# Kernel tuning notes

Hardware: AMD Instinct MI355X
Metric: run time of the kernel (lower is better)

The kernel has to match this reference:

```python
import jax, jax.numpy as jnp
import numpy as np

B, D_IN, D_H = 262144, 128, 128
PROJ_EPS = 1e-5  # ball projection epsilon (c = 1.0)


def _norm(x):
    return jnp.linalg.norm(x, axis=-1, keepdims=True)


def logmap0(x):
    # atanh(||x||) * x / ||x||, safe at 0 (c = 1)
    n = _norm(x)
    ns = jnp.where(n == 0, 0.5, n)
    return jnp.where(n == 0, jnp.zeros_like(x), jnp.arctanh(ns) * x / ns)


def expmap0(v):
    # tanh(||v||) * v / ||v||, safe at 0 (c = 1)
    n = _norm(v)
    ns = jnp.where(n == 0, 1.0, n)
    return jnp.where(n == 0, jnp.zeros_like(v), jnp.tanh(ns) * v / ns)


def proj(x):
    # clip back inside the unit Poincare ball
    n = _norm(x)
    maxnorm = 1.0 - PROJ_EPS
    ns = jnp.where(n == 0, 1.0, n)
    return jnp.where(n > maxnorm, x / ns * maxnorm, x)


def setup_inputs() -> dict:
    key = jax.random.key(0)
    ks = jax.random.split(key, 8)
    scale = 0.03  # keep points well inside the ball: ||x|| ~ 0.03*sqrt(128) ~ 0.34
    x = scale * jax.random.normal(ks[0], (B, D_IN), dtype=jnp.float32)
    h = scale * jax.random.normal(ks[1], (B, D_H), dtype=jnp.float32)
    fan_in = D_IN + D_H
    w_std = 1.0 / np.sqrt(fan_in)
    Wr = w_std * jax.random.normal(ks[2], (fan_in, D_H), dtype=jnp.float32)
    br = w_std * jax.random.normal(ks[3], (D_H,), dtype=jnp.float32)
    Wz = w_std * jax.random.normal(ks[4], (fan_in, D_H), dtype=jnp.float32)
    bz = w_std * jax.random.normal(ks[5], (D_H,), dtype=jnp.float32)
    Wh = w_std * jax.random.normal(ks[6], (fan_in, D_H), dtype=jnp.float32)
    bh = w_std * jax.random.normal(ks[7], (D_H,), dtype=jnp.float32)
    return {"x": x, "h": h, "Wr": Wr, "br": br, "Wz": Wz, "bz": bz, "Wh": Wh, "bh": bh}


def reference(x, h, Wr, br, Wz, bz, Wh, bh):
    x_tan = logmap0(x)            # [B, D_IN]
    h_tan = logmap0(h)            # [B, D_H]
    xh = jnp.concatenate([x_tan, h_tan], axis=1)  # [B, D_IN+D_H]
    r = jax.nn.sigmoid(xh @ Wr + br)
    z = jax.nn.sigmoid(xh @ Wz + bz)
    xh_reset = jnp.concatenate([x_tan, r * h_tan], axis=1)
    h_tilde = jnp.tanh(xh_reset @ Wh + bh)
    h_new_tan = (1.0 - z) * h_tan + z * h_tilde
    return proj(expmap0(h_new_tan))  # [B, D_H]
```

## Files before the change

kernel.cpp:

```cpp
#include <hip/hip_runtime.h>

typedef __attribute__((ext_vector_type(4))) float f32x4;
typedef __attribute__((ext_vector_type(8))) short bf16x8;
typedef __attribute__((ext_vector_type(4))) short bf16x4;

#define D 128
#define BM 64

__device__ __forceinline__ unsigned short f2bf(float f){
  union { float f; unsigned int i; } c; c.f = f;
  unsigned int i = c.i;
  i += 0x7fffu + ((i >> 16) & 1u);
  return (unsigned short)(i >> 16);
}
__device__ __forceinline__ float bf2f(unsigned short u){
  union { float f; unsigned int i; } c; c.i = ((unsigned int)u) << 16; return c.f;
}
__device__ __forceinline__ float sigmoid_f(float t){
  return 1.0f / (1.0f + __expf(-t));
}
__device__ __forceinline__ float tanh_f(float t){
  t = fminf(fmaxf(t, -20.0f), 20.0f);
  float e = __expf(2.0f * t);
  return (e - 1.0f) / (e + 1.0f);
}

__global__ void prep_weights(const float* __restrict__ Wr, const float* __restrict__ Wz,
                             const float* __restrict__ Wh, unsigned short* __restrict__ wp)
{
  int w = blockIdx.x >> 6;
  int f = blockIdx.x & 63;
  int l = threadIdx.x;
  const float* src = (w == 0) ? Wr : ((w == 1) ? Wz : Wh);
  int nf = f >> 3, kk = f & 7;
  int col = nf * 16 + (l & 15);
  int k0  = kk * 32 + (l >> 4) * 8;
  unsigned short* dst = wp + w * 32768 + (f * 64 + l) * 8;
#pragma unroll
  for (int j = 0; j < 8; ++j)
    dst[j] = f2bf(src[(k0 + j) * D + col]);
}

__global__ __launch_bounds__(256, 3) void gru_fused(
    const float* __restrict__ x, const float* __restrict__ h,
    const float* __restrict__ brp, const float* __restrict__ bzp, const float* __restrict__ bhp,
    const unsigned short* __restrict__ wp, float* __restrict__ out)
{
  __shared__ __align__(16) unsigned char SMEM[BM * 512 + BM * 256];
  unsigned char* A1 = SMEM;
  unsigned char* A2 = SMEM + BM * 512;
  float* HN = (float*)SMEM;

  const int tid = threadIdx.x;
  const int w   = tid >> 6;
  const int l   = tid & 63;
  const int l15 = l & 15;
  const int lq  = l >> 4;
  const size_t row0 = (size_t)blockIdx.x * BM;

  {
    const int row = tid >> 2;
    const int q   = tid & 3;
    const f32x4* xr = (const f32x4*)(x + (row0 + row) * D);
    const f32x4* hr = (const f32x4*)(h + (row0 + row) * D);
    f32x4 v[8];
    float ss = 0.f;
#pragma unroll
    for (int j = 0; j < 8; ++j){
      v[j] = xr[j * 4 + q];
      ss += v[j][0]*v[j][0] + v[j][1]*v[j][1] + v[j][2]*v[j][2] + v[j][3]*v[j][3];
    }
    ss += __shfl_xor(ss, 1, 64);
    ss += __shfl_xor(ss, 2, 64);
    float n = sqrtf(ss);
    float s = (n > 1e-20f) ? (0.5f * __logf((1.f + n) / (1.f - n)) / n) : 1.f;
#pragma unroll
    for (int j = 0; j < 8; ++j){
      unsigned int byte = (unsigned)(row * 512 + (4 * j + q) * 8) ^ (unsigned)((row & 7) << 4);
      bf16x4 pk;
      pk[0] = (short)f2bf(v[j][0] * s); pk[1] = (short)f2bf(v[j][1] * s);
      pk[2] = (short)f2bf(v[j][2] * s); pk[3] = (short)f2bf(v[j][3] * s);
      *(bf16x4*)(A1 + byte) = pk;
    }
    ss = 0.f;
#pragma unroll
    for (int j = 0; j < 8; ++j){
      v[j] = hr[j * 4 + q];
      ss += v[j][0]*v[j][0] + v[j][1]*v[j][1] + v[j][2]*v[j][2] + v[j][3]*v[j][3];
    }
    ss += __shfl_xor(ss, 1, 64);
    ss += __shfl_xor(ss, 2, 64);
    n = sqrtf(ss);
    s = (n > 1e-20f) ? (0.5f * __logf((1.f + n) / (1.f - n)) / n) : 1.f;
#pragma unroll
    for (int j = 0; j < 8; ++j){
      unsigned int byte = (unsigned)(row * 512 + 256 + (4 * j + q) * 8) ^ (unsigned)((row & 7) << 4);
      bf16x4 pk;
      pk[0] = (short)f2bf(v[j][0] * s); pk[1] = (short)f2bf(v[j][1] * s);
      pk[2] = (short)f2bf(v[j][2] * s); pk[3] = (short)f2bf(v[j][3] * s);
      *(bf16x4*)(A1 + byte) = pk;
    }
  }
  __syncthreads();

  const unsigned short* pwr = wp + w * 8192;
  const unsigned short* pwz = wp + 32768 + w * 8192;

  f32x4 accr0[4], accr1[4], accz0[4], accz1[4];
#pragma unroll
  for (int m = 0; m < 4; ++m){ accr0[m] = 0; accr1[m] = 0; accz0[m] = 0; accz1[m] = 0; }

#pragma unroll 2
  for (int kk = 0; kk < 8; ++kk){
    const bf16x8 br0f = *(const bf16x8*)(pwr + kk * 512 + l * 8);
    const bf16x8 br1f = *(const bf16x8*)(pwr + 4096 + kk * 512 + l * 8);
    const bf16x8 bz0f = *(const bf16x8*)(pwz + kk * 512 + l * 8);
    const bf16x8 bz1f = *(const bf16x8*)(pwz + 4096 + kk * 512 + l * 8);
#pragma unroll
    for (int m = 0; m < 4; ++m){
      const int row = m * 16 + l15;
      unsigned int byte = (unsigned)(row * 512 + (kk * 32 + lq * 8) * 2) ^ (unsigned)((row & 7) << 4);
      const bf16x8 a = *(const bf16x8*)(A1 + byte);
      accr0[m] = __builtin_amdgcn_mfma_f32_16x16x32_bf16(a, br0f, accr0[m], 0, 0, 0);
      accr1[m] = __builtin_amdgcn_mfma_f32_16x16x32_bf16(a, br1f, accr1[m], 0, 0, 0);
      accz0[m] = __builtin_amdgcn_mfma_f32_16x16x32_bf16(a, bz0f, accz0[m], 0, 0, 0);
      accz1[m] = __builtin_amdgcn_mfma_f32_16x16x32_bf16(a, bz1f, accz1[m], 0, 0, 0);
    }
  }

  const int cb = w * 32 + l15;
  const float br0v = brp[cb], br1v = brp[cb + 16];
  const float bz0v = bzp[cb], bz1v = bzp[cb + 16];
  f32x4 zk0[4], zk1[4];
#pragma unroll
  for (int m = 0; m < 4; ++m){
#pragma unroll
    for (int reg = 0; reg < 4; ++reg){
      const int row = m * 16 + lq * 4 + reg;
      const unsigned int swz = (unsigned)((row & 7) << 4);
      {
        float rv = sigmoid_f(accr0[m][reg] + br0v);
        zk0[m][reg] = sigmoid_f(accz0[m][reg] + bz0v);
        float ht = bf2f(*(const unsigned short*)(A1 + ((unsigned)(row * 512 + (128 + cb) * 2) ^ swz)));
        *(unsigned short*)(A2 + ((unsigned)(row * 256 + cb * 2) ^ swz)) = f2bf(rv * ht);
      }
      {
        float rv = sigmoid_f(accr1[m][reg] + br1v);
        zk1[m][reg] = sigmoid_f(accz1[m][reg] + bz1v);
        float ht = bf2f(*(const unsigned short*)(A1 + ((unsigned)(row * 512 + (128 + cb + 16) * 2) ^ swz)));
        *(unsigned short*)(A2 + ((unsigned)(row * 256 + (cb + 16) * 2) ^ swz)) = f2bf(rv * ht);
      }
    }
  }
  __syncthreads();

  const unsigned short* pwh = wp + 65536 + w * 8192;
  f32x4 ac0[4], ac1[4];
#pragma unroll
  for (int m = 0; m < 4; ++m){ ac0[m] = 0; ac1[m] = 0; }

#pragma unroll 2
  for (int kk = 0; kk < 4; ++kk){
    const bf16x8 b0 = *(const bf16x8*)(pwh + kk * 512 + l * 8);
    const bf16x8 b1 = *(const bf16x8*)(pwh + 4096 + kk * 512 + l * 8);
#pragma unroll
    for (int m = 0; m < 4; ++m){
      const int row = m * 16 + l15;
      unsigned int byte = (unsigned)(row * 512 + (kk * 32 + lq * 8) * 2) ^ (unsigned)((row & 7) << 4);
      const bf16x8 a = *(const bf16x8*)(A1 + byte);
      ac0[m] = __builtin_amdgcn_mfma_f32_16x16x32_bf16(a, b0, ac0[m], 0, 0, 0);
      ac1[m] = __builtin_amdgcn_mfma_f32_16x16x32_bf16(a, b1, ac1[m], 0, 0, 0);
    }
  }
#pragma unroll 2
  for (int kk = 4; kk < 8; ++kk){
    const bf16x8 b0 = *(const bf16x8*)(pwh + kk * 512 + l * 8);
    const bf16x8 b1 = *(const bf16x8*)(pwh + 4096 + kk * 512 + l * 8);
#pragma unroll
    for (int m = 0; m < 4; ++m){
      const int row = m * 16 + l15;
      unsigned int byte = (unsigned)(row * 256 + ((kk - 4) * 32 + lq * 8) * 2) ^ (unsigned)((row & 7) << 4);
      const bf16x8 a = *(const bf16x8*)(A2 + byte);
      ac0[m] = __builtin_amdgcn_mfma_f32_16x16x32_bf16(a, b0, ac0[m], 0, 0, 0);
      ac1[m] = __builtin_amdgcn_mfma_f32_16x16x32_bf16(a, b1, ac1[m], 0, 0, 0);
    }
  }

  const float bh0v = bhp[cb], bh1v = bhp[cb + 16];
  f32x4 hn0[4], hn1[4];
#pragma unroll
  for (int m = 0; m < 4; ++m){
#pragma unroll
    for (int reg = 0; reg < 4; ++reg){
      const int row = m * 16 + lq * 4 + reg;
      const unsigned int swz = (unsigned)((row & 7) << 4);
      {
        float htld = tanh_f(ac0[m][reg] + bh0v);
        float ht = bf2f(*(const unsigned short*)(A1 + ((unsigned)(row * 512 + (128 + cb) * 2) ^ swz)));
        float zv = zk0[m][reg];
        hn0[m][reg] = (1.f - zv) * ht + zv * htld;
      }
      {
        float htld = tanh_f(ac1[m][reg] + bh1v);
        float ht = bf2f(*(const unsigned short*)(A1 + ((unsigned)(row * 512 + (128 + cb + 16) * 2) ^ swz)));
        float zv = zk1[m][reg];
        hn1[m][reg] = (1.f - zv) * ht + zv * htld;
      }
    }
  }
  __syncthreads();

#pragma unroll
  for (int m = 0; m < 4; ++m){
#pragma unroll
    for (int reg = 0; reg < 4; ++reg){
      const int row = m * 16 + lq * 4 + reg;
      HN[row * 132 + cb]      = hn0[m][reg];
      HN[row * 132 + cb + 16] = hn1[m][reg];
    }
  }
  __syncthreads();

  {
    const int row = tid >> 2;
    const int q   = tid & 3;
    f32x4 v[8];
    float ss = 0.f;
#pragma unroll
    for (int j = 0; j < 8; ++j){
      v[j] = *(const f32x4*)(HN + row * 132 + (4 * j + q) * 4);
      ss += v[j][0]*v[j][0] + v[j][1]*v[j][1] + v[j][2]*v[j][2] + v[j][3]*v[j][3];
    }
    ss += __shfl_xor(ss, 1, 64);
    ss += __shfl_xor(ss, 2, 64);
    float n = sqrtf(ss);
    float sc = 1.f;
    if (n > 1e-20f){
      float th = tanh_f(n);
      th = fminf(th, 0.99999f);
      sc = th / n;
    }
    f32x4* op = (f32x4*)(out + (row0 + row) * D);
#pragma unroll
    for (int j = 0; j < 8; ++j){
      op[j * 4 + q] = v[j] * sc;
    }
  }
}

extern "C" void kernel_launch(void* const* d_in, const int* in_sizes, int n_in,
                              void* d_out, int out_size, void* d_ws, size_t ws_size,
                              hipStream_t stream)
{
  const float* x   = (const float*)d_in[0];
  const float* h   = (const float*)d_in[1];
  const float* Wr  = (const float*)d_in[2];
  const float* brp = (const float*)d_in[3];
  const float* Wz  = (const float*)d_in[4];
  const float* bzp = (const float*)d_in[5];
  const float* Wh  = (const float*)d_in[6];
  const float* bhp = (const float*)d_in[7];
  unsigned short* wsp = (unsigned short*)d_ws;

  prep_weights<<<192, 64, 0, stream>>>(Wr, Wz, Wh, wsp);
  gru_fused<<<262144 / BM, 256, 0, stream>>>(x, h, brp, bzp, bhp, wsp, (float*)d_out);
}
```

Measured before the change: 145.7 us.

## Shrink LDS by reusing h_tan slot for r*h and computing norms in-register

Drops the separate A2 buffer by writing r*h_tan back into the h_tan half of A1, with h_tan kept packed in registers for the final blend. The GEMM over Wh becomes a single 8-step loop over A1. The output norm is computed with cross-lane shuffles and a small LDS partial-sum array instead of staging the whole tile. Launch bounds rise to 4 blocks per SM to exploit the smaller LDS footprint. In exchange, register pressure increases and the output is written as scattered scalar stores rather than vectorized f32x4 rows.

```diff
diff --git a/kernel.cpp b/kernel.cpp
--- a/kernel.cpp
+++ b/kernel.cpp
@@ -41,15 +41,13 @@
     dst[j] = f2bf(src[(k0 + j) * D + col]);
 }
 
-__global__ __launch_bounds__(256, 3) void gru_fused(
+__global__ __launch_bounds__(256, 4) void gru_fused(
     const float* __restrict__ x, const float* __restrict__ h,
     const float* __restrict__ brp, const float* __restrict__ bzp, const float* __restrict__ bhp,
     const unsigned short* __restrict__ wp, float* __restrict__ out)
 {
-  __shared__ __align__(16) unsigned char SMEM[BM * 512 + BM * 256];
-  unsigned char* A1 = SMEM;
-  unsigned char* A2 = SMEM + BM * 512;
-  float* HN = (float*)SMEM;
+  __shared__ __align__(16) unsigned char A1[BM * 512];
+  float* P = (float*)A1;
 
   const int tid = threadIdx.x;
   const int w   = tid >> 6;
@@ -132,24 +130,35 @@
   const float br0v = brp[cb], br1v = brp[cb + 16];
   const float bz0v = bzp[cb], bz1v = bzp[cb + 16];
   f32x4 zk0[4], zk1[4];
+  unsigned int htp[4][4];
+  unsigned int rhp[4][4];
 #pragma unroll
   for (int m = 0; m < 4; ++m){
 #pragma unroll
     for (int reg = 0; reg < 4; ++reg){
       const int row = m * 16 + lq * 4 + reg;
       const unsigned int swz = (unsigned)((row & 7) << 4);
-      {
-        float rv = sigmoid_f(accr0[m][reg] + br0v);
-        zk0[m][reg] = sigmoid_f(accz0[m][reg] + bz0v);
-        float ht = bf2f(*(const unsigned short*)(A1 + ((unsigned)(row * 512 + (128 + cb) * 2) ^ swz)));
-        *(unsigned short*)(A2 + ((unsigned)(row * 256 + cb * 2) ^ swz)) = f2bf(rv * ht);
-      }
-      {
-        float rv = sigmoid_f(accr1[m][reg] + br1v);
-        zk1[m][reg] = sigmoid_f(accz1[m][reg] + bz1v);
-        float ht = bf2f(*(const unsigned short*)(A1 + ((unsigned)(row * 512 + (128 + cb + 16) * 2) ^ swz)));
-        *(unsigned short*)(A2 + ((unsigned)(row * 256 + (cb + 16) * 2) ^ swz)) = f2bf(rv * ht);
-      }
+      unsigned int u0 = *(const unsigned short*)(A1 + ((unsigned)(row * 512 + (128 + cb) * 2) ^ swz));
+      unsigned int u1 = *(const unsigned short*)(A1 + ((unsigned)(row * 512 + (128 + cb + 16) * 2) ^ swz));
+      htp[m][reg] = u0 | (u1 << 16);
+      float rv0 = sigmoid_f(accr0[m][reg] + br0v);
+      float rv1 = sigmoid_f(accr1[m][reg] + br1v);
+      zk0[m][reg] = sigmoid_f(accz0[m][reg] + bz0v);
+      zk1[m][reg] = sigmoid_f(accz1[m][reg] + bz1v);
+      rhp[m][reg] = (unsigned int)f2bf(rv0 * bf2f((unsigned short)u0))
+                  | ((unsigned int)f2bf(rv1 * bf2f((unsigned short)u1)) << 16);
+    }
+  }
+  __syncthreads();
+
+#pragma unroll
+  for (int m = 0; m < 4; ++m){
+#pragma unroll
+    for (int reg = 0; reg < 4; ++reg){
+      const int row = m * 16 + lq * 4 + reg;
+      const unsigned int swz = (unsigned)((row & 7) << 4);
+      *(unsigned short*)(A1 + ((unsigned)(row * 512 + (128 + cb) * 2) ^ swz))      = (unsigned short)(rhp[m][reg] & 0xffffu);
+      *(unsigned short*)(A1 + ((unsigned)(row * 512 + (128 + cb + 16) * 2) ^ swz)) = (unsigned short)(rhp[m][reg] >> 16);
     }
   }
   __syncthreads();
@@ -160,7 +169,7 @@
   for (int m = 0; m < 4; ++m){ ac0[m] = 0; ac1[m] = 0; }
 
 #pragma unroll 2
-  for (int kk = 0; kk < 4; ++kk){
+  for (int kk = 0; kk < 8; ++kk){
     const bf16x8 b0 = *(const bf16x8*)(pwh + kk * 512 + l * 8);
     const bf16x8 b1 = *(const bf16x8*)(pwh + 4096 + kk * 512 + l * 8);
 #pragma unroll
@@ -172,78 +181,56 @@
       ac1[m] = __builtin_amdgcn_mfma_f32_16x16x32_bf16(a, b1, ac1[m], 0, 0, 0);
     }
   }
-#pragma unroll 2
-  for (int kk = 4; kk < 8; ++kk){
-    const bf16x8 b0 = *(const bf16x8*)(pwh + kk * 512 + l * 8);
-    const bf16x8 b1 = *(const bf16x8*)(pwh + 4096 + kk * 512 + l * 8);
-#pragma unroll
-    for (int m = 0; m < 4; ++m){
-      const int row = m * 16 + l15;
-      unsigned int byte = (unsigned)(row * 256 + ((kk - 4) * 32 + lq * 8) * 2) ^ (unsigned)((row & 7) << 4);
-      const bf16x8 a = *(const bf16x8*)(A2 + byte);
-      ac0[m] = __builtin_amdgcn_mfma_f32_16x16x32_bf16(a, b0, ac0[m], 0, 0, 0);
-      ac1[m] = __builtin_amdgcn_mfma_f32_16x16x32_bf16(a, b1, ac1[m], 0, 0, 0);
-    }
-  }
 
   const float bh0v = bhp[cb], bh1v = bhp[cb + 16];
-  f32x4 hn0[4], hn1[4];
-#pragma unroll
-  for (int m = 0; m < 4; ++m){
-#pragma unroll
-    for (int reg = 0; reg < 4; ++reg){
-      const int row = m * 16 + lq * 4 + reg;
-      const unsigned int swz = (unsigned)((row & 7) << 4);
-      {
-        float htld = tanh_f(ac0[m][reg] + bh0v);
-        float ht = bf2f(*(const unsigned short*)(A1 + ((unsigned)(row * 512 + (128 + cb) * 2) ^ swz)));
-        float zv = zk0[m][reg];
-        hn0[m][reg] = (1.f - zv) * ht + zv * htld;
+  f32x4 o0[4], o1[4];
+#pragma unroll
+  for (int m = 0; m < 4; ++m){
+#pragma unroll
+    for (int reg = 0; reg < 4; ++reg){
+      float htld0 = tanh_f(ac0[m][reg] + bh0v);
+      float htld1 = tanh_f(ac1[m][reg] + bh1v);
+      float ht0 = bf2f((unsigned short)(htp[m][reg] & 0xffffu));
+      float ht1 = bf2f((unsigned short)(htp[m][reg] >> 16));
+      float z0 = zk0[m][reg], z1 = zk1[m][reg];
+      o0[m][reg] = (1.f - z0) * ht0 + z0 * htld0;
+      o1[m][reg] = (1.f - z1) * ht1 + z1 * htld1;
+    }
+  }
+  __syncthreads();
+
+#pragma unroll
+  for (int m = 0; m < 4; ++m){
+#pragma unroll
+    for (int reg = 0; reg < 4; ++reg){
+      const int row = m * 16 + lq * 4 + reg;
+      float s = o0[m][reg] * o0[m][reg] + o1[m][reg] * o1[m][reg];
+      s += __shfl_xor(s, 1, 16);
+      s += __shfl_xor(s, 2, 16);
+      s += __shfl_xor(s, 4, 16);
+      s += __shfl_xor(s, 8, 16);
+      if (l15 == 0) P[row * 4 + w] = s;
+    }
+  }
+  __syncthreads();
+
+#pragma unroll
+  for (int m = 0; m < 4; ++m){
+#pragma unroll
+    for (int reg = 0; reg < 4; ++reg){
+      const int row = m * 16 + lq * 4 + reg;
+      const f32x4 p4 = *(const f32x4*)(P + row * 4);
+      float ss = p4[0] + p4[1] + p4[2] + p4[3];
+      float n = sqrtf(ss);
+      float sc = 1.f;
+      if (n > 1e-20f){
+        float th = tanh_f(n);
+        th = fminf(th, 0.99999f);
+        sc = th / n;
       }
-      {
-        float htld = tanh_f(ac1[m][reg] + bh1v);
-        float ht = bf2f(*(const unsigned short*)(A1 + ((unsigned)(row * 512 + (128 + cb + 16) * 2) ^ swz)));
-        float zv = zk1[m][reg];
-        hn1[m][reg] = (1.f - zv) * ht + zv * htld;
-      }
-    }
-  }
-  __syncthreads();
-
-#pragma unroll
-  for (int m = 0; m < 4; ++m){
-#pragma unroll
-    for (int reg = 0; reg < 4; ++reg){
-      const int row = m * 16 + lq * 4 + reg;
-      HN[row * 132 + cb]      = hn0[m][reg];
-      HN[row * 132 + cb + 16] = hn1[m][reg];
-    }
-  }
-  __syncthreads();
-
-  {
-    const int row = tid >> 2;
-    const int q   = tid & 3;
-    f32x4 v[8];
-    float ss = 0.f;
-#pragma unroll
-    for (int j = 0; j < 8; ++j){
-      v[j] = *(const f32x4*)(HN + row * 132 + (4 * j + q) * 4);
-      ss += v[j][0]*v[j][0] + v[j][1]*v[j][1] + v[j][2]*v[j][2] + v[j][3]*v[j][3];
-    }
-    ss += __shfl_xor(ss, 1, 64);
-    ss += __shfl_xor(ss, 2, 64);
-    float n = sqrtf(ss);
-    float sc = 1.f;
-    if (n > 1e-20f){
-      float th = tanh_f(n);
-      th = fminf(th, 0.99999f);
-      sc = th / n;
-    }
-    f32x4* op = (f32x4*)(out + (row0 + row) * D);
-#pragma unroll
-    for (int j = 0; j < 8; ++j){
-      op[j * 4 + q] = v[j] * sc;
+      float* orow = out + (row0 + row) * D;
+      orow[cb]      = o0[m][reg] * sc;
+      orow[cb + 16] = o1[m][reg] * sc;
     }
   }
 }
```

New measurement: 185.2 us. 1.27x slower.
